# Kernel optimization log

Measured on AMD Instinct MI355X. Metric: run time of the kernel, lower is better.

The kernel has to match this reference:

```python
import jax, jax.numpy as jnp
import numpy as np

N_HEADS = 16
D_MODEL = 1024
TOTAL = 8192
N_SEQ = 8
SEQ_LEN = TOTAL // N_SEQ


def setup_inputs() -> dict:
    key = jax.random.key(0)
    ks = jax.random.split(key, 12)
    f = jnp.float32
    d = D_MODEL
    inp = {
        "query": jax.random.normal(ks[0], (TOTAL, d), f),
        "key": jax.random.normal(ks[1], (TOTAL, d), f),
        "value": jax.random.normal(ks[2], (TOTAL, d), f),
        "seq_lengths_q": jnp.full((N_SEQ,), SEQ_LEN, jnp.int64 if jax.config.jax_enable_x64 else jnp.int32),
        "seq_lengths_kv": jnp.full((N_SEQ,), SEQ_LEN, jnp.int64 if jax.config.jax_enable_x64 else jnp.int32),
        "Wq": jax.random.normal(ks[3], (d, d), f) * 0.02,
        "bq": jnp.zeros((d,), f),
        "Wk": jax.random.normal(ks[4], (d, d), f) * 0.02,
        "bk": jnp.zeros((d,), f),
        "Wv": jax.random.normal(ks[5], (d, d), f) * 0.02,
        "bv": jnp.zeros((d,), f),
        "Wo": jax.random.normal(ks[6], (d, d), f) * 0.02,
        "bo": jnpp if False else jnp.zeros((d,), f),
    }
    return inp


def reference(query, key, value, seq_lengths_q, seq_lengths_kv, Wq, bq, Wk, bk, Wv, bv, Wo, bo):
    Tq, d = query.shape
    Tkv = key.shape[0]
    H = N_HEADS
    Dh = d // H
    B = seq_lengths_q.shape[0]
    Lq = Tq // B  # equal-length packed sequences
    Lkv = Tkv // B
    scale = 1.0 / jnp.sqrt(jnp.asarray(Dh, query.dtype))

    # torch Linear: x @ W.T + b
    Q = (query @ Wq.T + bq).reshape(H, Tq, Dh)   # NOTE: raw view, no transpose
    K = (key @ Wk.T + bk).reshape(H, Tkv, Dh)    # (replicates original's view semantics)
    V = (value @ Wv.T + bv).reshape(H, Tkv, Dh)

    # Block-diagonal mask over equal-length sequences == per-block attention.
    Qb = Q.reshape(H, B, Lq, Dh)
    Kb = K.reshape(H, B, Lkv, Dh)
    Vb = V.reshape(H, B, Lkv, Dh)

    scores = jnp.einsum("hbqd,hbkd->hbqk", Qb, Kb) * scale  # [H,B,Lq,Lkv]
    probs = jax.nn.softmax(scores, axis=-1)
    attn = jnp.einsum("hbqk,hbkd->hbqd", probs, Vb)          # [H,B,Lq,Dh]

    attn = attn.reshape(H, Tq, Dh).reshape(Tq, d)  # matches .view(total_q, d_model)
    out = attn @ Wo.T + bo
    return out
```

## Files before the change

kernel.cpp:

```cpp
#include <hip/hip_runtime.h>
#include <hip/hip_bf16.h>

#define TOTAL   8192
#define DMODEL  1024
#define NHEADS  16
#define NSEQ    8
#define DH      64

typedef float  f32x4 __attribute__((ext_vector_type(4)));
typedef short  s16x8 __attribute__((ext_vector_type(8)));
typedef unsigned short u16;
typedef u16    u16x8 __attribute__((ext_vector_type(8)));

__device__ __forceinline__ u16 f2bf_rne(float x) {
  union { float f; unsigned u; } v; v.f = x;
  unsigned r = v.u + 0x7FFFu + ((v.u >> 16) & 1u);
  return (u16)(r >> 16);
}

__device__ __forceinline__ void async_cp16(const u16* g, u16* l) {
  __builtin_amdgcn_global_load_lds(
      (const __attribute__((address_space(1))) unsigned int*)g,
      (__attribute__((address_space(3))) unsigned int*)l, 16, 0, 0);
}

__device__ __forceinline__ void cvt8_one(const float* __restrict__ src,
                                         u16* __restrict__ dst, long i) {
  float4 a = *reinterpret_cast<const float4*>(src + i);
  float4 b = *reinterpret_cast<const float4*>(src + i + 4);
  u16x8 o;
  o[0] = f2bf_rne(a.x); o[1] = f2bf_rne(a.y); o[2] = f2bf_rne(a.z); o[3] = f2bf_rne(a.w);
  o[4] = f2bf_rne(b.x); o[5] = f2bf_rne(b.y); o[6] = f2bf_rne(b.z); o[7] = f2bf_rne(b.w);
  *reinterpret_cast<u16x8*>(dst + i) = o;
}

__global__ __launch_bounds__(256) void cvt8(const float* __restrict__ src,
                                            u16* __restrict__ dst) {
  cvt8_one(src, dst, ((long)blockIdx.x * 256 + threadIdx.x) * 8);
}

__global__ __launch_bounds__(256) void cvt8_w4(const float* __restrict__ w0,
                                               const float* __restrict__ w1,
                                               const float* __restrict__ w2,
                                               const float* __restrict__ w3,
                                               u16* __restrict__ dst) {
  const float* srcs[4] = {w0, w1, w2, w3};
  cvt8_one(srcs[blockIdx.y], dst + (long)blockIdx.y * (DMODEL * (long)DMODEL),
           ((long)blockIdx.x * 256 + threadIdx.x) * 8);
}

__global__ __launch_bounds__(256) void cvt8_x3(const float* __restrict__ x0,
                                               const float* __restrict__ x1,
                                               const float* __restrict__ x2,
                                               u16* __restrict__ dst) {
  const float* srcs[3] = {x0, x1, x2};
  cvt8_one(srcs[blockIdx.y], dst + (long)blockIdx.y * (TOTAL * (long)DMODEL),
           ((long)blockIdx.x * 256 + threadIdx.x) * 8);
}

template<bool OUT_BF16>
__device__ __forceinline__ void gemm256_core(const u16* __restrict__ A,
                                             const u16* __restrict__ B,
                                             const float* __restrict__ bias,
                                             void* __restrict__ Cp,
                                             long bm0, long bn0, u16* lds) {
  const int tid  = threadIdx.x;
  const int lane = tid & 63;
  const int wv   = tid >> 6;
  const int quad = lane >> 4;
  const int m16  = lane & 15;
  const int wm   = (wv >> 1) * 64;
  const int wn   = (wv & 1) * 64;

  const int l8   = lane >> 3;
  const int slot = (lane & 7) ^ l8;
  const long g_lane = (long)l8 * DMODEL + slot * 8;
  const u16* Ap = A + (bm0 + wv * 32) * (long)DMODEL + g_lane;
  const u16* Bp = B + (bn0 + wv * 16) * (long)DMODEL + g_lane;
  u16* ldsA = lds + wv * (4 * 512);
  u16* ldsB = lds + 16384 + wv * (2 * 512);

  const int swz0 = ((quad * 16)      ^ ((m16 & 7) << 4)) >> 1;
  const int swz1 = ((64 + quad * 16) ^ ((m16 & 7) << 4)) >> 1;
  const int aro = (wm + m16) * 64;
  const int bro = 16384 + (wn + m16) * 64;

  f32x4 acc[4][4] = {};

#define STAGE_A(buf, kt) do {                                       \
    _Pragma("unroll")                                               \
    for (int al = 0; al < 4; al++)                                  \
      async_cp16(Ap + (long)(kt) * 64 + al * (8 * DMODEL),          \
                 ldsA + (buf) * 24576 + al * 512);                  \
  } while (0)
#define STAGE_B(buf, kt) do {                                       \
    _Pragma("unroll")                                               \
    for (int bl = 0; bl < 2; bl++)                                  \
      async_cp16(Bp + (long)(kt) * 64 + bl * (8 * DMODEL),          \
                 ldsB + (buf) * 24576 + bl * 512);                  \
  } while (0)

  STAGE_A(0, 0); STAGE_B(0, 0);
  STAGE_A(1, 1); STAGE_B(1, 1);

  #pragma unroll
  for (int t = 0; t < 16; t++) {
    const int cur = t % 3;
    const int stg = (t + 2) % 3;
    if (t < 15) asm volatile("s_waitcnt vmcnt(6)" ::: "memory");
    else        asm volatile("s_waitcnt vmcnt(0)" ::: "memory");
    __builtin_amdgcn_s_barrier();
    asm volatile("" ::: "memory");

    const u16* lb = lds + cur * 24576;

    if (t < 14) STAGE_A(stg, t + 2);
    s16x8 bf[4][2], af[2][2];
    #pragma unroll
    for (int n = 0; n < 4; n++) {
      bf[n][0] = *(const s16x8*)&lb[bro + n * 1024 + swz0];
      bf[n][1] = *(const s16x8*)&lb[bro + n * 1024 + swz1];
    }
    #pragma unroll
    for (int i = 0; i < 2; i++) {
      af[i][0] = *(const s16x8*)&lb[aro + i * 1024 + swz0];
      af[i][1] = *(const s16x8*)&lb[aro + i * 1024 + swz1];
    }
    asm volatile("s_waitcnt lgkmcnt(0)" ::: "memory");
    __builtin_amdgcn_sched_barrier(0);
    __builtin_amdgcn_s_setprio(1);
    #pragma unroll
    for (int i = 0; i < 2; i++)
      #pragma unroll
      for (int n = 0; n < 4; n++) {
        acc[i][n] = __builtin_amdgcn_mfma_f32_16x16x32_bf16(af[i][0], bf[n][0], acc[i][n], 0, 0, 0);
        acc[i][n] = __builtin_amdgcn_mfma_f32_16x16x32_bf16(af[i][1], bf[n][1], acc[i][n], 0, 0, 0);
      }
    __builtin_amdgcn_s_setprio(0);
    __builtin_amdgcn_s_barrier();

    if (t < 14) STAGE_B(stg, t + 2);
    s16x8 ag[2][2];
    #pragma unroll
    for (int i = 0; i < 2; i++) {
      ag[i][0] = *(const s16x8*)&lb[aro + (i + 2) * 1024 + swz0];
      ag[i][1] = *(const s16x8*)&lb[aro + (i + 2) * 1024 + swz1];
    }
    asm volatile("s_waitcnt lgkmcnt(0)" ::: "memory");
    __builtin_amdgcn_sched_barrier(0);
    __builtin_amdgcn_s_setprio(1);
    #pragma unroll
    for (int i = 0; i < 2; i++)
      #pragma unroll
      for (int n = 0; n < 4; n++) {
        acc[i + 2][n] = __builtin_amdgcn_mfma_f32_16x16x32_bf16(ag[i][0], bf[n][0], acc[i + 2][n], 0, 0, 0);
        acc[i + 2][n] = __builtin_amdgcn_mfma_f32_16x16x32_bf16(ag[i][1], bf[n][1], acc[i + 2][n], 0, 0, 0);
      }
    __builtin_amdgcn_s_setprio(0);
  }
#undef STAGE_A
#undef STAGE_B

  #pragma unroll
  for (int n = 0; n < 4; n++) {
    const long col = bn0 + wn + n * 16 + m16;
    const float bj = bias[col];
    #pragma unroll
    for (int i = 0; i < 4; i++) {
      const long row0 = bm0 + wm + i * 16 + quad * 4;
      #pragma unroll
      for (int r = 0; r < 4; r++) {
        float v = acc[i][n][r] + bj;
        if constexpr (OUT_BF16)
          ((u16*)Cp)[(row0 + r) * DMODEL + col] = f2bf_rne(v);
        else
          ((float*)Cp)[(row0 + r) * DMODEL + col] = v;
      }
    }
  }
}

__device__ __forceinline__ void decode_wg(int x, long& bm0, long& bn0) {
  const int wg = (x & 7) * 32 + (x >> 3);
  bm0 = (long)(wg >> 3) * 256;
  bn0 = (long)(wg & 7) * 128;
}

template<bool OUT_BF16>
__global__ __launch_bounds__(512, 2) void gemm256_nt(const u16* __restrict__ A,
                                                     const u16* __restrict__ B,
                                                     const float* __restrict__ bias,
                                                     void* __restrict__ Cp) {
  __shared__ __align__(1024) u16 lds[3 * 24576];
  long bm0, bn0;
  decode_wg(blockIdx.x, bm0, bn0);
  gemm256_core<OUT_BF16>(A, B, bias, Cp, bm0, bn0, lds);
}

__global__ __launch_bounds__(512, 2) void gemm256_qkv(const u16* __restrict__ X3,
                                                      const u16* __restrict__ W3,
                                                      const float* __restrict__ bq,
                                                      const float* __restrict__ bk,
                                                      const float* __restrict__ bv,
                                                      u16* __restrict__ QKV) {
  __shared__ __align__(1024) u16 lds[3 * 24576];
  const int z = blockIdx.y;
  const float* bias = (z == 0) ? bq : (z == 1) ? bk : bv;
  long bm0, bn0;
  decode_wg(blockIdx.x, bm0, bn0);
  gemm256_core<true>(X3 + (long)z * (TOTAL * (long)DMODEL),
                     W3 + (long)z * (DMODEL * (long)DMODEL),
                     bias,
                     QKV + (long)z * (TOTAL * (long)DMODEL),
                     bm0, bn0, lds);
}

__global__ __launch_bounds__(256) void transpose_v(const u16* __restrict__ Vbf,
                                                   u16* __restrict__ Vt) {
  constexpr int TP = 72;
  __shared__ u16 tile[64 * TP];
  const int tid = threadIdx.x;
  const long base = (long)blockIdx.y * 65536;
  const int kt = blockIdx.x;
  {
    int k = tid >> 2, dh0 = (tid & 3) * 16;
    const u16* g = Vbf + base + (long)(kt * 64 + k) * 64 + dh0;
    u16x8 a = ((const u16x8*)g)[0];
    u16x8 b = ((const u16x8*)g)[1];
    #pragma unroll
    for (int i = 0; i < 8; i++) tile[(dh0 + i) * TP + k] = a[i];
    #pragma unroll
    for (int i = 0; i < 8; i++) tile[(dh0 + 8 + i) * TP + k] = b[i];
  }
  __syncthreads();
  {
    int dh = tid >> 2, k0 = (tid & 3) * 16;
    u16x8 a = *(const u16x8*)&tile[dh * TP + k0];
    u16x8 b = *(const u16x8*)&tile[dh * TP + k0 + 8];
    u16* g = Vt + base + (long)dh * 1024 + kt * 64 + k0;
    ((u16x8*)g)[0] = a;
    ((u16x8*)g)[1] = b;
  }
}

__global__ __launch_bounds__(256) void attn_kernel(const u16* __restrict__ Qbf,
                                                   const u16* __restrict__ Kbf,
                                                   const u16* __restrict__ Vt,
                                                   u16* __restrict__ Obf) {
  constexpr int KP = 72;
  __shared__ u16 Ks[64 * KP];
  __shared__ u16 Vs[64 * KP];
  __shared__ u16 Es[4 * 32 * KP];
  const int tid  = threadIdx.x;
  const int lane = tid & 63;
  const int wv   = tid >> 6;
  const int quad = lane >> 4;
  const int m16  = lane & 15;
  const int qt   = blockIdx.y;
  const long base = (long)blockIdx.x * 65536;

  const int qrow0 = qt * 128 + wv * 32;
  s16x8 aq[2][2];
  #pragma unroll
  for (int g = 0; g < 2; g++)
    #pragma unroll
    for (int s = 0; s < 2; s++)
      aq[g][s] = *(const s16x8*)(Qbf + base + (long)(qrow0 + g * 16 + m16) * 64 + s * 32 + quad * 8);

  f32x4 acc_o[2][4] = {};
  f32x4 acc_d[2] = {};

  union { u16x8 u; s16x8 s; } onesu;
  u16 ov = (m16 == 0) ? (u16)0x3F80 : (u16)0;
  #pragma unroll
  for (int i = 0; i < 8; i++) onesu.u[i] = ov;
  const s16x8 bones = onesu.s;

  const float SC = 0.125f * 1.44269504088896340736f;
  const int sr = tid >> 2;
  const int sk = (tid & 3) * 16;

  for (int nt = 0; nt < 16; nt++) {
    {
      const u16* g = Kbf + base + nt * 4096 + (long)sr * 64 + sk;
      u16x8 a = ((const u16x8*)g)[0];
      u16x8 b = ((const u16x8*)g)[1];
      *(u16x8*)&Ks[sr * KP + sk]     = a;
      *(u16x8*)&Ks[sr * KP + sk + 8] = b;
    }
    {
      const u16* g = Vt + base + (long)sr * 1024 + nt * 64 + sk;
      u16x8 a = ((const u16x8*)g)[0];
      u16x8 b = ((const u16x8*)g)[1];
      *(u16x8*)&Vs[sr * KP + sk]     = a;
      *(u16x8*)&Vs[sr * KP + sk + 8] = b;
    }
    __syncthreads();

    #pragma unroll
    for (int n = 0; n < 4; n++) {
      s16x8 bk0 = *(const s16x8*)&Ks[(n * 16 + m16) * KP + quad * 8];
      s16x8 bk1 = *(const s16x8*)&Ks[(n * 16 + m16) * KP + 32 + quad * 8];
      #pragma unroll
      for (int g = 0; g < 2; g++) {
        f32x4 s = {0.f, 0.f, 0.f, 0.f};
        s = __builtin_amdgcn_mfma_f32_16x16x32_bf16(aq[g][0], bk0, s, 0, 0, 0);
        s = __builtin_amdgcn_mfma_f32_16x16x32_bf16(aq[g][1], bk1, s, 0, 0, 0);
        #pragma unroll
        for (int r = 0; r < 4; r++) {
          float e = __builtin_amdgcn_exp2f(s[r] * SC);
          Es[(wv * 32 + g * 16 + quad * 4 + r) * KP + n * 16 + m16] = f2bf_rne(e);
        }
      }
    }
    s16x8 ae[2][2];
    #pragma unroll
    for (int g = 0; g < 2; g++) {
      ae[g][0] = *(const s16x8*)&Es[(wv * 32 + g * 16 + m16) * KP + quad * 8];
      ae[g][1] = *(const s16x8*)&Es[(wv * 32 + g * 16 + m16) * KP + 32 + quad * 8];
    }
    #pragma unroll
    for (int n = 0; n < 4; n++) {
      s16x8 bv0 = *(const s16x8*)&Vs[(n * 16 + m16) * KP + quad * 8];
      s16x8 bv1 = *(const s16x8*)&Vs[(n * 16 + m16) * KP + 32 + quad * 8];
      #pragma unroll
      for (int g = 0; g < 2; g++) {
        acc_o[g][n] = __builtin_amdgcn_mfma_f32_16x16x32_bf16(ae[g][0], bv0, acc_o[g][n], 0, 0, 0);
        acc_o[g][n] = __builtin_amdgcn_mfma_f32_16x16x32_bf16(ae[g][1], bv1, acc_o[g][n], 0, 0, 0);
      }
    }
    #pragma unroll
    for (int g = 0; g < 2; g++) {
      acc_d[g] = __builtin_amdgcn_mfma_f32_16x16x32_bf16(ae[g][0], bones, acc_d[g], 0, 0, 0);
      acc_d[g] = __builtin_amdgcn_mfma_f32_16x16x32_bf16(ae[g][1], bones, acc_d[g], 0, 0, 0);
    }
    __syncthreads();
  }

  #pragma unroll
  for (int g = 0; g < 2; g++)
    #pragma unroll
    for (int r = 0; r < 4; r++) {
      float d = __shfl(acc_d[g][r], lane & 48);
      float rinv = 1.0f / d;
      const long orow = base + (long)(qrow0 + g * 16 + quad * 4 + r) * 64;
      #pragma unroll
      for (int n = 0; n < 4; n++)
        Obf[orow + n * 16 + m16] = f2bf_rne(acc_o[g][n][r] * rinv);
    }
}

extern "C" void kernel_launch(void* const* d_in, const int* in_sizes, int n_in,
                              void* d_out, int out_size, void* d_ws, size_t ws_size,
                              hipStream_t stream) {
  const float* query = (const float*)d_in[0];
  const float* key_  = (const float*)d_in[1];
  const float* value = (const float*)d_in[2];
  const float* Wq = (const float*)d_in[5];
  const float* bq = (const float*)d_in[6];
  const float* Wk = (const float*)d_in[7];
  const float* bk = (const float*)d_in[8];
  const float* Wv = (const float*)d_in[9];
  const float* bv = (const float*)d_in[10];
  const float* Wo = (const float*)d_in[11];
  const float* bo = (const float*)d_in[12];

  char* ws = (char*)d_ws;
  const size_t FUSED_NEED = 104ull << 20;

  if (ws_size >= FUSED_NEED) {
    u16* Wbf = (u16*)(ws);
    u16* QKV = (u16*)(ws + (8l << 20));
    u16* Qbf = QKV;
    u16* Kbf = QKV + 1 * (TOTAL * (long)DMODEL);
    u16* Vbf = QKV + 2 * (TOTAL * (long)DMODEL);
    u16* X3  = (u16*)(ws + (56l << 20));
    u16* Vt  = X3;
    u16* Obf = Vbf;

    cvt8_w4<<<dim3(512, 4), 256, 0, stream>>>(Wq, Wk, Wv, Wo, Wbf);
    cvt8_x3<<<dim3(4096, 3), 256, 0, stream>>>(query, key_, value, X3);
    gemm256_qkv<<<dim3(256, 3), 512, 0, stream>>>(X3, Wbf, bq, bk, bv, QKV);
    transpose_v<<<dim3(16, 128), 256, 0, stream>>>(Vbf, Vt);
    attn_kernel<<<dim3(128, 8), 256, 0, stream>>>(Qbf, Kbf, Vt, Obf);
    gemm256_nt<false><<<dim3(256), 512, 0, stream>>>(Obf, Wbf + 3 * 1048576, bo, (float*)d_out);
  } else {
    u16* Wbf = (u16*)(ws);
    u16* Xbf = (u16*)(ws + (8l << 20));
    u16* Qbf = (u16*)(ws + (24l << 20));
    u16* Kbf = (u16*)(ws + (40l << 20));
    u16* Vbf = (u16*)(ws + (56l << 20));
    u16* Vt  = Xbf;
    u16* Obf = Vbf;

    cvt8_w4<<<dim3(512, 4), 256, 0, stream>>>(Wq, Wk, Wv, Wo, Wbf);
    cvt8<<<4096, 256, 0, stream>>>(query, Xbf);
    gemm256_nt<true><<<dim3(256), 512, 0, stream>>>(Xbf, Wbf + 0 * 1048576, bq, Qbf);
    cvt8<<<4096, 256, 0, stream>>>(key_, Xbf);
    gemm256_nt<true><<<dim3(256), 512, 0, stream>>>(Xbf, Wbf + 1 * 1048576, bk, Kbf);
    cvt8<<<4096, 256, 0, stream>>>(value, Xbf);
    gemm256_nt<true><<<dim3(256), 512, 0, stream>>>(Xbf, Wbf + 2 * 1048576, bv, Vbf);
    transpose_v<<<dim3(16, 128), 256, 0, stream>>>(Vbf, Vt);
    attn_kernel<<<dim3(128, 8), 256, 0, stream>>>(Qbf, Kbf, Vt, Obf);
    gemm256_nt<false><<<dim3(256), 512, 0, stream>>>(Obf, Wbf + 3 * 1048576, bo, (float*)d_out);
  }
}
```

Measured before the change: 307.0 us.

## Prefetch K/V tiles into registers and transpose score MFMA for packed exp stores

Global loads of the next K and V tiles are issued into registers right after the barrier, so they overlap with the current tile's compute instead of stalling before the LDS store. The score MFMA operands are swapped so each lane holds four consecutive key columns. This lets the four bf16 exponentials be packed into one 64-bit LDS store instead of four scalar stores. It also adds an explicit lgkmcnt wait with a sched barrier, plus s_setprio around the PV MFMAs, in exchange for higher register pressure from the prefetch buffers.

```diff
diff --git a/kernel.cpp b/kernel.cpp
--- a/kernel.cpp
+++ b/kernel.cpp
@@ -11,6 +11,7 @@
 typedef short  s16x8 __attribute__((ext_vector_type(8)));
 typedef unsigned short u16;
 typedef u16    u16x8 __attribute__((ext_vector_type(8)));
+typedef unsigned u32x2 __attribute__((ext_vector_type(2)));
 
 __device__ __forceinline__ u16 f2bf_rne(float x) {
   union { float f; unsigned u; } v; v.f = x;
@@ -280,45 +281,54 @@
   const int sr = tid >> 2;
   const int sk = (tid & 3) * 16;
 
+  const u16* gK = Kbf + base + (long)sr * 64 + sk;
+  const u16* gV = Vt  + base + (long)sr * 1024 + sk;
+  u16x8 kra = ((const u16x8*)gK)[0], krb = ((const u16x8*)gK)[1];
+  u16x8 vra = ((const u16x8*)gV)[0], vrb = ((const u16x8*)gV)[1];
+
   for (int nt = 0; nt < 16; nt++) {
-    {
-      const u16* g = Kbf + base + nt * 4096 + (long)sr * 64 + sk;
-      u16x8 a = ((const u16x8*)g)[0];
-      u16x8 b = ((const u16x8*)g)[1];
-      *(u16x8*)&Ks[sr * KP + sk]     = a;
-      *(u16x8*)&Ks[sr * KP + sk + 8] = b;
-    }
-    {
-      const u16* g = Vt + base + (long)sr * 1024 + nt * 64 + sk;
-      u16x8 a = ((const u16x8*)g)[0];
-      u16x8 b = ((const u16x8*)g)[1];
-      *(u16x8*)&Vs[sr * KP + sk]     = a;
-      *(u16x8*)&Vs[sr * KP + sk + 8] = b;
-    }
+    *(u16x8*)&Ks[sr * KP + sk]     = kra;
+    *(u16x8*)&Ks[sr * KP + sk + 8] = krb;
+    *(u16x8*)&Vs[sr * KP + sk]     = vra;
+    *(u16x8*)&Vs[sr * KP + sk + 8] = vrb;
     __syncthreads();
-
-    #pragma unroll
-    for (int n = 0; n < 4; n++) {
-      s16x8 bk0 = *(const s16x8*)&Ks[(n * 16 + m16) * KP + quad * 8];
-      s16x8 bk1 = *(const s16x8*)&Ks[(n * 16 + m16) * KP + 32 + quad * 8];
+    if (nt < 15) {
+      const u16* nK = gK + (nt + 1) * 4096;
+      const u16* nV = gV + (nt + 1) * 64;
+      kra = ((const u16x8*)nK)[0]; krb = ((const u16x8*)nK)[1];
+      vra = ((const u16x8*)nV)[0]; vrb = ((const u16x8*)nV)[1];
+    }
+
+    #pragma unroll
+    for (int mt = 0; mt < 4; mt++) {
+      const int krow = (mt * 16 + m16) * KP;
+      s16x8 kf0 = *(const s16x8*)&Ks[krow + quad * 8];
+      s16x8 kf1 = *(const s16x8*)&Ks[krow + 32 + quad * 8];
       #pragma unroll
       for (int g = 0; g < 2; g++) {
         f32x4 s = {0.f, 0.f, 0.f, 0.f};
-        s = __builtin_amdgcn_mfma_f32_16x16x32_bf16(aq[g][0], bk0, s, 0, 0, 0);
-        s = __builtin_amdgcn_mfma_f32_16x16x32_bf16(aq[g][1], bk1, s, 0, 0, 0);
-        #pragma unroll
-        for (int r = 0; r < 4; r++) {
-          float e = __builtin_amdgcn_exp2f(s[r] * SC);
-          Es[(wv * 32 + g * 16 + quad * 4 + r) * KP + n * 16 + m16] = f2bf_rne(e);
-        }
+        s = __builtin_amdgcn_mfma_f32_16x16x32_bf16(kf0, aq[g][0], s, 0, 0, 0);
+        s = __builtin_amdgcn_mfma_f32_16x16x32_bf16(kf1, aq[g][1], s, 0, 0, 0);
+        float e0 = __builtin_amdgcn_exp2f(s[0] * SC);
+        float e1 = __builtin_amdgcn_exp2f(s[1] * SC);
+        float e2 = __builtin_amdgcn_exp2f(s[2] * SC);
+        float e3 = __builtin_amdgcn_exp2f(s[3] * SC);
+        unsigned p0 = (unsigned)f2bf_rne(e0) | ((unsigned)f2bf_rne(e1) << 16);
+        unsigned p1 = (unsigned)f2bf_rne(e2) | ((unsigned)f2bf_rne(e3) << 16);
+        u32x2 w; w.x = p0; w.y = p1;
+        *(u32x2*)&Es[(wv * 32 + g * 16 + m16) * KP + mt * 16 + quad * 4] = w;
       }
     }
+    asm volatile("s_waitcnt lgkmcnt(0)" ::: "memory");
+    __builtin_amdgcn_sched_barrier(0);
+
     s16x8 ae[2][2];
     #pragma unroll
     for (int g = 0; g < 2; g++) {
       ae[g][0] = *(const s16x8*)&Es[(wv * 32 + g * 16 + m16) * KP + quad * 8];
       ae[g][1] = *(const s16x8*)&Es[(wv * 32 + g * 16 + m16) * KP + 32 + quad * 8];
     }
+    __builtin_amdgcn_s_setprio(1);
     #pragma unroll
     for (int n = 0; n < 4; n++) {
       s16x8 bv0 = *(const s16x8*)&Vs[(n * 16 + m16) * KP + quad * 8];
@@ -334,6 +344,7 @@
       acc_d[g] = __builtin_amdgcn_mfma_f32_16x16x32_bf16(ae[g][0], bones, acc_d[g], 0, 0, 0);
       acc_d[g] = __builtin_amdgcn_mfma_f32_16x16x32_bf16(ae[g][1], bones, acc_d[g], 0, 0, 0);
     }
+    __builtin_amdgcn_s_setprio(0);
     __syncthreads();
   }
 
```

Measured after the change: 318.6 us. 1.04x slower.
